# Kernel optimization log

Hardware: AMD Instinct MI355X
Metric: run time of the kernel (lower is better)

The kernel has to match this reference:

```python
import jax, jax.numpy as jnp
import numpy as np

N_USERS, N_ITEMS, N_GENRES = 31360, 6807, 18
TOTAL = N_USERS + N_ITEMS + N_GENRES          # 38185
OFFSET = TOTAL - N_GENRES                      # 38167
D = 16                                         # embedding_dim
B = 524288                                     # batch
MLP_DIMS = [64, 32, 16]
IN_DIM = 3 * D                                 # field_num * embedding_dim


def setup_inputs() -> dict:
    key = jax.random.key(0)
    ks = jax.random.split(key, 14)
    user = jax.random.randint(ks[0], (B, 1), 0, N_USERS)
    item = N_USERS + jax.random.randint(ks[1], (B, 1), 0, N_ITEMS)
    x_onehot = jnp.concatenate([user, item], axis=1)            # [B,2] global ids
    multi_hot = jax.random.randint(ks[2], (B, N_GENRES), 0, 2)  # [B,18] 0/1 mask
    s = 0.05
    emb_table = s * jax.random.normal(ks[3], (TOTAL, D), jnp.float32)
    fc_table = s * jax.random.normal(ks[4], (TOTAL, 1), jnp.float32)
    W1 = s * jax.random.normal(ks[5], (IN_DIM, MLP_DIMS[0]), jnp.float32)
    b1 = jnp.zeros((MLP_DIMS[0],), jnp.float32)
    W2 = s * jax.random.normal(ks[6], (MLP_DIMS[0], MLP_DIMS[1]), jnp.float32)
    b2 = jnp.zeros((MLP_DIMS[1],), jnp.float32)
    W3 = s * jax.random.normal(ks[7], (MLP_DIMS[1], MLP_DIMS[2]), jnp.float32)
    b3 = jnp.zeros((MLP_DIMS[2],), jnp.float32)
    W4 = s * jax.random.normal(ks[8], (MLP_DIMS[2], 1), jnp.float32)
    b4 = jnp.zeros((1,), jnp.float32)
    bias = jnp.zeros((1,), jnp.float32)
    return {"x_onehot": x_onehot, "multi_hot": multi_hot,
            "emb_table": emb_table, "fc_table": fc_table,
            "W1": W1, "b1": b1, "W2": W2, "b2": b2,
            "W3": W3, "b3": b3, "W4": W4, "b4": b4, "bias": bias}


def reference(x_onehot, multi_hot, emb_table, fc_table,
              W1, b1, W2, b2, W3, b3, W4, b4, bias):
    mh = multi_hot.astype(emb_table.dtype)                      # [B,18]
    # ragged multi-hot sum == mask @ genre slice of table (EmbeddingBag sum)
    embed_mh = mh @ emb_table[OFFSET:]                          # [B,D]
    embed_x = jnp.concatenate(
        [emb_table[x_onehot], embed_mh[:, None, :]], axis=1)    # [B,3,D]
    fc_mh = mh @ fc_table[OFFSET:]                              # [B,1]
    fc_x = jnp.concatenate(
        [fc_table[x_onehot], fc_mh[:, None, :]], axis=1)        # [B,3,1]
    # FM second-order term
    sum_e = embed_x.sum(axis=1)                                 # [B,D]
    fm_y = bias + fc_x.sum(axis=1) + 0.5 * jnp.sum(
        sum_e ** 2 - (embed_x ** 2).sum(axis=1), axis=1, keepdims=True)  # [B,1]
    # MLP (dropout inactive at inference)
    h = embed_x.reshape(embed_x.shape[0], -1)                   # [B,48]
    h = jax.nn.relu(h @ W1 + b1)
    h = jax.nn.relu(h @ W2 + b2)
    h = jax.nn.relu(h @ W3 + b3)
    mlp_y = h @ W4 + b4                                         # [B,1]
    return jax.nn.sigmoid(fm_y[:, 0] + mlp_y[:, 0])             # [B]
```

## Files before the change

kernel.cpp:

```cpp
#include <hip/hip_runtime.h>
#include <hip/hip_bf16.h>

namespace {

constexpr int kBatch  = 524288;
constexpr int kD      = 16;
constexpr int kOffset = 38167;
constexpr int kNG     = 18;
constexpr int kAStr   = 72;

constexpr int W1A  = 0;
constexpr int W1B  = 2560;
constexpr int W2O  = 5120;
constexpr int W3O  = 7424;
constexpr int WTOT = 8064;

typedef __attribute__((ext_vector_type(8))) short short8;
typedef __attribute__((ext_vector_type(4))) float f32x4;

__device__ __forceinline__ unsigned short f2bf(float f) {
    return __builtin_bit_cast(unsigned short, __float2bfloat16(f));
}
__device__ __forceinline__ unsigned pk2(float a, float b) {
    return (unsigned)f2bf(a) | ((unsigned)f2bf(b) << 16);
}
__device__ __forceinline__ float bf2f(unsigned short s) {
    union { unsigned u; float f; } v; v.u = ((unsigned)s) << 16;
    return v.f;
}

__global__ void prep_weights(const float* __restrict__ emb,
                             const float* __restrict__ W1,
                             const float* __restrict__ W2,
                             const float* __restrict__ W3,
                             unsigned short* __restrict__ wimg)
{
    const int t = (int)threadIdx.x;
    for (int i = t; i < WTOT; i += 256) wimg[i] = 0;
    __syncthreads();
    for (int i = t; i < 64 * 32; i += 256) {
        int n = i >> 5, k = i & 31;
        wimg[W1A + n * 40 + k] = f2bf(W1[k * 64 + n]);
    }
    for (int i = t; i < 512; i += 256) {
        int c = i >> 5, r = i & 31, g = r >> 3, j = r & 7;
        int k = 8 * g + j;
        wimg[W1A + (4 * c + g) * 40 + 32 + j] =
            (k < kNG) ? f2bf(emb[(size_t)(kOffset + k) * kD + c]) : (unsigned short)0;
    }
    for (int i = t; i < 64 * 16; i += 256) {
        int n = i >> 4, kk = i & 15;
        wimg[W1B + n * 40 + kk] = f2bf(W1[(32 + kk) * 64 + n]);
    }
    for (int i = t; i < 32 * 64; i += 256) {
        int n = i >> 6, k = i & 63;
        wimg[W2O + n * 72 + k] = f2bf(W2[k * 32 + n]);
    }
    for (int i = t; i < 16 * 32; i += 256) {
        int n = i >> 5, k = i & 31;
        wimg[W3O + n * 40 + k] = f2bf(W3[k * 16 + n]);
    }
}

__global__ __launch_bounds__(256, 3) void deepfm_fwd(
    const int*   __restrict__ x_onehot,
    const int*   __restrict__ multi_hot,
    const float* __restrict__ emb,
    const float* __restrict__ fc,
    const unsigned short* __restrict__ wimg,
    const float* __restrict__ b1,
    const float* __restrict__ b2,
    const float* __restrict__ b3,
    const float* __restrict__ W4,
    const float* __restrict__ b4,
    const float* __restrict__ bias,
    float*       __restrict__ out)
{
    __shared__ alignas(16) unsigned short s_w[WTOT];
    __shared__ alignas(16) unsigned short s_act[4][64 * kAStr];

    const int t = (int)threadIdx.x;

    {
        const uint4* src = reinterpret_cast<const uint4*>(wimg);
        uint4*       dst = reinterpret_cast<uint4*>(s_w);
        #pragma unroll
        for (int q = 0; q < 4; ++q) {
            const int idx = t + 256 * q;
            if (idx < WTOT / 8) dst[idx] = src[idx];
        }
    }

    const int i    = (int)blockIdx.x * 256 + t;
    const int lane = t & 63;
    const int w    = t >> 6;
    const int c    = lane & 15, g = lane >> 4;
    unsigned short* __restrict__ aw = s_act[w];
    unsigned short* __restrict__ ar = aw + lane * kAStr;

    int2 mh[9];
    {
        const int2* mh2 = reinterpret_cast<const int2*>(multi_hot + (size_t)kNG * i);
        #pragma unroll
        for (int q = 0; q < 9; ++q) mh[q] = mh2[q];
    }
    const int2 ids = *reinterpret_cast<const int2*>(x_onehot + 2 * (size_t)i);

    float h[32];
    {
        const float4* eu = reinterpret_cast<const float4*>(emb + (size_t)ids.x * kD);
        #pragma unroll
        for (int q = 0; q < 4; ++q) {
            const float4 a = eu[q];
            h[4*q+0] = a.x; h[4*q+1] = a.y; h[4*q+2] = a.z; h[4*q+3] = a.w;
        }
        const float4* ei = reinterpret_cast<const float4*>(emb + (size_t)ids.y * kD);
        #pragma unroll
        for (int q = 0; q < 4; ++q) {
            const float4 a = ei[q];
            h[16+4*q+0] = a.x; h[16+4*q+1] = a.y; h[16+4*q+2] = a.z; h[16+4*q+3] = a.w;
        }
    }

    float b1v[4];
    #pragma unroll
    for (int nt = 0; nt < 4; ++nt) b1v[nt] = b1[16 * nt + c];
    float b2v[2]; b2v[0] = b2[c]; b2v[1] = b2[16 + c];
    const float b3v = b3[c];

    float lin = bias[0] + b4[0] + fc[ids.x] + fc[ids.y];
    #pragma unroll
    for (int q = 0; q < 9; ++q) {
        lin += mh[q].x ? fc[kOffset + 2 * q]     : 0.f;
        lin += mh[q].y ? fc[kOffset + 2 * q + 1] : 0.f;
    }

    {
        unsigned mw[9];
        #pragma unroll
        for (int q = 0; q < 9; ++q)
            mw[q] = (mh[q].x ? 0x3F80u : 0u) | (mh[q].y ? 0x3F800000u : 0u);
        uint4 v0; v0.x = mw[0]; v0.y = mw[1]; v0.z = mw[2]; v0.w = mw[3];
        uint4 v1; v1.x = mw[4]; v1.y = mw[5]; v1.z = mw[6]; v1.w = mw[7];
        uint4 v2; v2.x = mw[8]; v2.y = 0u;    v2.z = 0u;    v2.w = 0u;
        uint4 vz; vz.x = vz.y = vz.z = vz.w = 0u;
        *reinterpret_cast<uint4*>(ar +  0) = v0;
        *reinterpret_cast<uint4*>(ar +  8) = v1;
        *reinterpret_cast<uint4*>(ar + 16) = v2;
        *reinterpret_cast<uint4*>(ar + 24) = vz;
        *reinterpret_cast<uint4*>(ar + 48) = vz;
        *reinterpret_cast<uint4*>(ar + 56) = vz;
    }

    __syncthreads();

    const f32x4 z4 = {0.f, 0.f, 0.f, 0.f};

    {
        const short8 bfrag = *reinterpret_cast<const short8*>(s_w + W1A + (4 * c + g) * 40 + 32);
        short8 af[4];
        #pragma unroll
        for (int mt = 0; mt < 4; ++mt)
            af[mt] = *reinterpret_cast<const short8*>(aw + (16 * mt + c) * kAStr + 8 * g);
        f32x4 accb[4];
        #pragma unroll
        for (int mt = 0; mt < 4; ++mt)
            accb[mt] = __builtin_amdgcn_mfma_f32_16x16x32_bf16(af[mt], bfrag, z4, 0, 0, 0);
        #pragma unroll
        for (int mt = 0; mt < 4; ++mt)
            #pragma unroll
            for (int r = 0; r < 4; ++r)
                aw[(16 * mt + 4 * g + r) * kAStr + 32 + c] = f2bf(accb[mt][r]);
    }

    {
        #pragma unroll
        for (int q = 0; q < 4; ++q) {
            uint4 d;
            d.x = pk2(h[8*q+0], h[8*q+1]);
            d.y = pk2(h[8*q+2], h[8*q+3]);
            d.z = pk2(h[8*q+4], h[8*q+5]);
            d.w = pk2(h[8*q+6], h[8*q+7]);
            *reinterpret_cast<uint4*>(ar + 8 * q) = d;
        }
    }

    float fm = 0.f;
    {
        const uint4 p0 = *reinterpret_cast<const uint4*>(ar + 32);
        const uint4 p1 = *reinterpret_cast<const uint4*>(ar + 40);
        const unsigned pp[8] = {p0.x, p0.y, p0.z, p0.w, p1.x, p1.y, p1.z, p1.w};
        float em[16];
        #pragma unroll
        for (int j = 0; j < 8; ++j) {
            em[2*j+0] = bf2f((unsigned short)(pp[j] & 0xFFFFu));
            em[2*j+1] = bf2f((unsigned short)(pp[j] >> 16));
        }
        #pragma unroll
        for (int d = 0; d < kD; ++d) fm = fmaf(h[d], h[16 + d], fm);
        #pragma unroll
        for (int d = 0; d < kD; ++d) fm = fmaf(h[d] + h[16 + d], em[d], fm);
    }

    f32x4 acc1[4][4];
    #pragma unroll
    for (int mt = 0; mt < 4; ++mt)
        #pragma unroll
        for (int nt = 0; nt < 4; ++nt) acc1[mt][nt] = z4;
    #pragma unroll
    for (int kt = 0; kt < 2; ++kt) {
        short8 af[4], bfr[4];
        #pragma unroll
        for (int mt = 0; mt < 4; ++mt)
            af[mt] = *reinterpret_cast<const short8*>(aw + (16*mt + c) * kAStr + 32*kt + 8*g);
        const int wb = kt ? W1B : W1A;
        #pragma unroll
        for (int nt = 0; nt < 4; ++nt)
            bfr[nt] = *reinterpret_cast<const short8*>(s_w + wb + (16*nt + c) * 40 + 8*g);
        #pragma unroll
        for (int mt = 0; mt < 4; ++mt)
            #pragma unroll
            for (int nt = 0; nt < 4; ++nt)
                acc1[mt][nt] = __builtin_amdgcn_mfma_f32_16x16x32_bf16(af[mt], bfr[nt], acc1[mt][nt], 0, 0, 0);
    }
    #pragma unroll
    for (int mt = 0; mt < 4; ++mt)
        #pragma unroll
        for (int nt = 0; nt < 4; ++nt)
            #pragma unroll
            for (int r = 0; r < 4; ++r) {
                const float v = fmaxf(acc1[mt][nt][r] + b1v[nt], 0.f);
                aw[(16*mt + 4*g + r) * kAStr + 16*nt + c] = f2bf(v);
            }

    f32x4 acc2[4][2];
    #pragma unroll
    for (int mt = 0; mt < 4; ++mt)
        #pragma unroll
        for (int nt = 0; nt < 2; ++nt) acc2[mt][nt] = z4;
    #pragma unroll
    for (int kt = 0; kt < 2; ++kt) {
        short8 af[4], bfr[2];
        #pragma unroll
        for (int mt = 0; mt < 4; ++mt)
            af[mt] = *reinterpret_cast<const short8*>(aw + (16*mt + c) * kAStr + 32*kt + 8*g);
        #pragma unroll
        for (int nt = 0; nt < 2; ++nt)
            bfr[nt] = *reinterpret_cast<const short8*>(s_w + W2O + (16*nt + c) * 72 + 32*kt + 8*g);
        #pragma unroll
        for (int mt = 0; mt < 4; ++mt)
            #pragma unroll
            for (int nt = 0; nt < 2; ++nt)
                acc2[mt][nt] = __builtin_amdgcn_mfma_f32_16x16x32_bf16(af[mt], bfr[nt], acc2[mt][nt], 0, 0, 0);
    }
    #pragma unroll
    for (int mt = 0; mt < 4; ++mt)
        #pragma unroll
        for (int nt = 0; nt < 2; ++nt)
            #pragma unroll
            for (int r = 0; r < 4; ++r) {
                const float v = fmaxf(acc2[mt][nt][r] + b2v[nt], 0.f);
                aw[(16*mt + 4*g + r) * kAStr + 16*nt + c] = f2bf(v);
            }

    f32x4 acc3[4];
    #pragma unroll
    for (int mt = 0; mt < 4; ++mt) acc3[mt] = z4;
    {
        const short8 bfr = *reinterpret_cast<const short8*>(s_w + W3O + c * 40 + 8*g);
        short8 af[4];
        #pragma unroll
        for (int mt = 0; mt < 4; ++mt)
            af[mt] = *reinterpret_cast<const short8*>(aw + (16*mt + c) * kAStr + 8*g);
        #pragma unroll
        for (int mt = 0; mt < 4; ++mt)
            acc3[mt] = __builtin_amdgcn_mfma_f32_16x16x32_bf16(af[mt], bfr, acc3[mt], 0, 0, 0);
    }
    #pragma unroll
    for (int mt = 0; mt < 4; ++mt)
        #pragma unroll
        for (int r = 0; r < 4; ++r) {
            const float v = fmaxf(acc3[mt][r] + b3v, 0.f);
            aw[(16*mt + 4*g + r) * kAStr + c] = f2bf(v);
        }

    float mlp = 0.f;
    {
        const uint4 p0 = *reinterpret_cast<const uint4*>(ar);
        const uint4 p1 = *reinterpret_cast<const uint4*>(ar + 8);
        const unsigned pp[8] = {p0.x, p0.y, p0.z, p0.w, p1.x, p1.y, p1.z, p1.w};
        #pragma unroll
        for (int j = 0; j < 8; ++j) {
            mlp = fmaf(bf2f((unsigned short)(pp[j] & 0xFFFFu)), W4[2*j],     mlp);
            mlp = fmaf(bf2f((unsigned short)(pp[j] >> 16)),     W4[2*j + 1], mlp);
        }
    }

    const float x = lin + fm + mlp;
    out[i] = 1.0f / (1.0f + __expf(-x));
}

}

extern "C" void kernel_launch(void* const* d_in, const int* in_sizes, int n_in,
                              void* d_out, int out_size, void* d_ws, size_t ws_size,
                              hipStream_t stream) {
    (void)in_sizes; (void)n_in; (void)ws_size; (void)out_size;
    const int*   x_onehot  = (const int*)  d_in[0];
    const int*   multi_hot = (const int*)  d_in[1];
    const float* emb       = (const float*)d_in[2];
    const float* fc        = (const float*)d_in[3];
    const float* W1        = (const float*)d_in[4];
    const float* b1        = (const float*)d_in[5];
    const float* W2        = (const float*)d_in[6];
    const float* b2        = (const float*)d_in[7];
    const float* W3        = (const float*)d_in[8];
    const float* b3        = (const float*)d_in[9];
    const float* W4        = (const float*)d_in[10];
    const float* b4        = (const float*)d_in[11];
    const float* biasp     = (const float*)d_in[12];
    float* out = (float*)d_out;
    unsigned short* wimg = (unsigned short*)d_ws;

    hipLaunchKernelGGL(prep_weights, dim3(1), dim3(256), 0, stream,
                       emb, W1, W2, W3, wimg);
    hipLaunchKernelGGL(deepfm_fwd, dim3(kBatch / 256), dim3(256), 0, stream,
                       x_onehot, multi_hot, emb, fc, wimg,
                       b1, b2, b3, W4, b4, biasp, out);
}
```

Before: 37.36 us.

## Swizzle LDS layouts with XOR and move to 512-thread blocks

Replaces the padded-stride shared-memory layout for activations and weights with a 128-byte-row XOR-swizzled layout to avoid bank conflicts on the MFMA fragment loads and the scattered accumulator stores. The block size doubles to 512 threads (8 waves), which spreads the per-block weight copy over twice as many rows. Bias-add and ReLU are rewritten on float2 vectors so they can use packed instructions. LDS per block grows to about 78KB, so the occupancy target of 4 blocks may not be reachable, and the swizzle adds address arithmetic.

```diff
diff --git a/kernel.cpp b/kernel.cpp
--- a/kernel.cpp
+++ b/kernel.cpp
@@ -7,16 +7,16 @@
 constexpr int kD      = 16;
 constexpr int kOffset = 38167;
 constexpr int kNG     = 18;
-constexpr int kAStr   = 72;
-
-constexpr int W1A  = 0;
-constexpr int W1B  = 2560;
-constexpr int W2O  = 5120;
-constexpr int W3O  = 7424;
-constexpr int WTOT = 8064;
+
+constexpr int W1B0   = 0;
+constexpr int W2B0   = 8192;
+constexpr int W3B0   = 12288;
+constexpr int GB0    = 13312;
+constexpr int WBYTES = 14336;
 
 typedef __attribute__((ext_vector_type(8))) short short8;
 typedef __attribute__((ext_vector_type(4))) float f32x4;
+typedef __attribute__((ext_vector_type(2))) float f32x2;
 
 __device__ __forceinline__ unsigned short f2bf(float f) {
     return __builtin_bit_cast(unsigned short, __float2bfloat16(f));
@@ -27,6 +27,12 @@
 __device__ __forceinline__ float bf2f(unsigned short s) {
     union { unsigned u; float f; } v; v.u = ((unsigned)s) << 16;
     return v.f;
+}
+__device__ __forceinline__ unsigned short* AP(unsigned short* b, int row, int col) {
+    return (unsigned short*)((char*)b + row * 128 + ((col * 2) ^ ((row & 7) << 4)));
+}
+__device__ __forceinline__ const unsigned short* APc(const unsigned short* b, int row, int col) {
+    return (const unsigned short*)((const char*)b + row * 128 + ((col * 2) ^ ((row & 7) << 4)));
 }
 
 __global__ void prep_weights(const float* __restrict__ emb,
@@ -36,33 +42,32 @@
                              unsigned short* __restrict__ wimg)
 {
     const int t = (int)threadIdx.x;
-    for (int i = t; i < WTOT; i += 256) wimg[i] = 0;
+    for (int i = t; i < WBYTES / 2; i += 256) wimg[i] = 0;
     __syncthreads();
+    for (int i = t; i < 48 * 64; i += 256) {
+        int k = i >> 6, n = i & 63;
+        int byte = W1B0 + n * 128 + ((k * 2) ^ ((n & 7) << 4));
+        wimg[byte >> 1] = f2bf(W1[k * 64 + n]);
+    }
     for (int i = t; i < 64 * 32; i += 256) {
-        int n = i >> 5, k = i & 31;
-        wimg[W1A + n * 40 + k] = f2bf(W1[k * 64 + n]);
+        int k = i >> 5, n = i & 31;
+        int byte = W2B0 + n * 128 + ((k * 2) ^ ((n & 7) << 4));
+        wimg[byte >> 1] = f2bf(W2[k * 32 + n]);
+    }
+    for (int i = t; i < 32 * 16; i += 256) {
+        int k = i >> 4, n = i & 15;
+        int byte = W3B0 + n * 64 + ((k * 2) ^ ((n & 3) << 4));
+        wimg[byte >> 1] = f2bf(W3[k * 16 + n]);
     }
     for (int i = t; i < 512; i += 256) {
         int c = i >> 5, r = i & 31, g = r >> 3, j = r & 7;
-        int k = 8 * g + j;
-        wimg[W1A + (4 * c + g) * 40 + 32 + j] =
-            (k < kNG) ? f2bf(emb[(size_t)(kOffset + k) * kD + c]) : (unsigned short)0;
-    }
-    for (int i = t; i < 64 * 16; i += 256) {
-        int n = i >> 4, kk = i & 15;
-        wimg[W1B + n * 40 + kk] = f2bf(W1[(32 + kk) * 64 + n]);
-    }
-    for (int i = t; i < 32 * 64; i += 256) {
-        int n = i >> 6, k = i & 63;
-        wimg[W2O + n * 72 + k] = f2bf(W2[k * 32 + n]);
-    }
-    for (int i = t; i < 16 * 32; i += 256) {
-        int n = i >> 5, k = i & 31;
-        wimg[W3O + n * 40 + k] = f2bf(W3[k * 16 + n]);
-    }
-}
-
-__global__ __launch_bounds__(256, 3) void deepfm_fwd(
+        int kg = 8 * g + j;
+        wimg[(GB0 >> 1) + (4 * c + g) * 8 + j] =
+            (kg < kNG) ? f2bf(emb[(size_t)(kOffset + kg) * kD + c]) : (unsigned short)0;
+    }
+}
+
+__global__ __launch_bounds__(512, 4) void deepfm_fwd(
     const int*   __restrict__ x_onehot,
     const int*   __restrict__ multi_hot,
     const float* __restrict__ emb,
@@ -76,27 +81,24 @@
     const float* __restrict__ bias,
     float*       __restrict__ out)
 {
-    __shared__ alignas(16) unsigned short s_w[WTOT];
-    __shared__ alignas(16) unsigned short s_act[4][64 * kAStr];
+    __shared__ alignas(16) unsigned short s_w[WBYTES / 2];
+    __shared__ alignas(16) unsigned short s_act[8 * 4096];
 
     const int t = (int)threadIdx.x;
 
     {
         const uint4* src = reinterpret_cast<const uint4*>(wimg);
         uint4*       dst = reinterpret_cast<uint4*>(s_w);
-        #pragma unroll
-        for (int q = 0; q < 4; ++q) {
-            const int idx = t + 256 * q;
-            if (idx < WTOT / 8) dst[idx] = src[idx];
-        }
-    }
-
-    const int i    = (int)blockIdx.x * 256 + t;
+        if (t < 896) dst[t] = src[t];
+        const int t2 = t + 512;
+        if (t2 < 896) dst[t2] = src[t2];
+    }
+
+    const int i    = (int)blockIdx.x * 512 + t;
     const int lane = t & 63;
     const int w    = t >> 6;
     const int c    = lane & 15, g = lane >> 4;
-    unsigned short* __restrict__ aw = s_act[w];
-    unsigned short* __restrict__ ar = aw + lane * kAStr;
+    unsigned short* __restrict__ aw = s_act + w * 4096;
 
     int2 mh[9];
     {
@@ -144,24 +146,25 @@
         uint4 v1; v1.x = mw[4]; v1.y = mw[5]; v1.z = mw[6]; v1.w = mw[7];
         uint4 v2; v2.x = mw[8]; v2.y = 0u;    v2.z = 0u;    v2.w = 0u;
         uint4 vz; vz.x = vz.y = vz.z = vz.w = 0u;
-        *reinterpret_cast<uint4*>(ar +  0) = v0;
-        *reinterpret_cast<uint4*>(ar +  8) = v1;
-        *reinterpret_cast<uint4*>(ar + 16) = v2;
-        *reinterpret_cast<uint4*>(ar + 24) = vz;
-        *reinterpret_cast<uint4*>(ar + 48) = vz;
-        *reinterpret_cast<uint4*>(ar + 56) = vz;
+        *reinterpret_cast<uint4*>(AP(aw, lane,  0)) = v0;
+        *reinterpret_cast<uint4*>(AP(aw, lane,  8)) = v1;
+        *reinterpret_cast<uint4*>(AP(aw, lane, 16)) = v2;
+        *reinterpret_cast<uint4*>(AP(aw, lane, 24)) = vz;
+        *reinterpret_cast<uint4*>(AP(aw, lane, 48)) = vz;
+        *reinterpret_cast<uint4*>(AP(aw, lane, 56)) = vz;
     }
 
     __syncthreads();
 
     const f32x4 z4 = {0.f, 0.f, 0.f, 0.f};
-
-    {
-        const short8 bfrag = *reinterpret_cast<const short8*>(s_w + W1A + (4 * c + g) * 40 + 32);
+    const f32x2 zz = {0.f, 0.f};
+
+    {
+        const short8 bfrag = *reinterpret_cast<const short8*>(s_w + (GB0 >> 1) + (4 * c + g) * 8);
         short8 af[4];
         #pragma unroll
         for (int mt = 0; mt < 4; ++mt)
-            af[mt] = *reinterpret_cast<const short8*>(aw + (16 * mt + c) * kAStr + 8 * g);
+            af[mt] = *reinterpret_cast<const short8*>(APc(aw, 16 * mt + c, 8 * g));
         f32x4 accb[4];
         #pragma unroll
         for (int mt = 0; mt < 4; ++mt)
@@ -170,7 +173,7 @@
         for (int mt = 0; mt < 4; ++mt)
             #pragma unroll
             for (int r = 0; r < 4; ++r)
-                aw[(16 * mt + 4 * g + r) * kAStr + 32 + c] = f2bf(accb[mt][r]);
+                *AP(aw, 16 * mt + 4 * g + r, 32 + c) = f2bf(accb[mt][r]);
     }
 
     {
@@ -181,14 +184,14 @@
             d.y = pk2(h[8*q+2], h[8*q+3]);
             d.z = pk2(h[8*q+4], h[8*q+5]);
             d.w = pk2(h[8*q+6], h[8*q+7]);
-            *reinterpret_cast<uint4*>(ar + 8 * q) = d;
+            *reinterpret_cast<uint4*>(AP(aw, lane, 8 * q)) = d;
         }
     }
 
     float fm = 0.f;
     {
-        const uint4 p0 = *reinterpret_cast<const uint4*>(ar + 32);
-        const uint4 p1 = *reinterpret_cast<const uint4*>(ar + 40);
+        const uint4 p0 = *reinterpret_cast<const uint4*>(APc(aw, lane, 32));
+        const uint4 p1 = *reinterpret_cast<const uint4*>(APc(aw, lane, 40));
         const unsigned pp[8] = {p0.x, p0.y, p0.z, p0.w, p1.x, p1.y, p1.z, p1.w};
         float em[16];
         #pragma unroll
@@ -212,11 +215,11 @@
         short8 af[4], bfr[4];
         #pragma unroll
         for (int mt = 0; mt < 4; ++mt)
-            af[mt] = *reinterpret_cast<const short8*>(aw + (16*mt + c) * kAStr + 32*kt + 8*g);
-        const int wb = kt ? W1B : W1A;
+            af[mt] = *reinterpret_cast<const short8*>(APc(aw, 16*mt + c, 32*kt + 8*g));
         #pragma unroll
         for (int nt = 0; nt < 4; ++nt)
-            bfr[nt] = *reinterpret_cast<const short8*>(s_w + wb + (16*nt + c) * 40 + 8*g);
+            bfr[nt] = *reinterpret_cast<const short8*>(
+                (const char*)s_w + W1B0 + (16*nt + c) * 128 + ((64*kt + 16*g) ^ ((c & 7) << 4)));
         #pragma unroll
         for (int mt = 0; mt < 4; ++mt)
             #pragma unroll
@@ -226,12 +229,18 @@
     #pragma unroll
     for (int mt = 0; mt < 4; ++mt)
         #pragma unroll
-        for (int nt = 0; nt < 4; ++nt)
-            #pragma unroll
-            for (int r = 0; r < 4; ++r) {
-                const float v = fmaxf(acc1[mt][nt][r] + b1v[nt], 0.f);
-                aw[(16*mt + 4*g + r) * kAStr + 16*nt + c] = f2bf(v);
-            }
+        for (int nt = 0; nt < 4; ++nt) {
+            f32x2 p0 = {acc1[mt][nt][0], acc1[mt][nt][1]};
+            f32x2 p1 = {acc1[mt][nt][2], acc1[mt][nt][3]};
+            const f32x2 bb = {b1v[nt], b1v[nt]};
+            p0 += bb; p1 += bb;
+            p0 = __builtin_elementwise_max(p0, zz);
+            p1 = __builtin_elementwise_max(p1, zz);
+            *AP(aw, 16*mt + 4*g + 0, 16*nt + c) = f2bf(p0[0]);
+            *AP(aw, 16*mt + 4*g + 1, 16*nt + c) = f2bf(p0[1]);
+            *AP(aw, 16*mt + 4*g + 2, 16*nt + c) = f2bf(p1[0]);
+            *AP(aw, 16*mt + 4*g + 3, 16*nt + c) = f2bf(p1[1]);
+        }
 
     f32x4 acc2[4][2];
     #pragma unroll
@@ -243,10 +252,11 @@
         short8 af[4], bfr[2];
         #pragma unroll
         for (int mt = 0; mt < 4; ++mt)
-            af[mt] = *reinterpret_cast<const short8*>(aw + (16*mt + c) * kAStr + 32*kt + 8*g);
+            af[mt] = *reinterpret_cast<const short8*>(APc(aw, 16*mt + c, 32*kt + 8*g));
         #pragma unroll
         for (int nt = 0; nt < 2; ++nt)
-            bfr[nt] = *reinterpret_cast<const short8*>(s_w + W2O + (16*nt + c) * 72 + 32*kt + 8*g);
+            bfr[nt] = *reinterpret_cast<const short8*>(
+                (const char*)s_w + W2B0 + (16*nt + c) * 128 + ((64*kt + 16*g) ^ ((c & 7) << 4)));
         #pragma unroll
         for (int mt = 0; mt < 4; ++mt)
             #pragma unroll
@@ -256,38 +266,51 @@
     #pragma unroll
     for (int mt = 0; mt < 4; ++mt)
         #pragma unroll
-        for (int nt = 0; nt < 2; ++nt)
-            #pragma unroll
-            for (int r = 0; r < 4; ++r) {
-                const float v = fmaxf(acc2[mt][nt][r] + b2v[nt], 0.f);
-                aw[(16*mt + 4*g + r) * kAStr + 16*nt + c] = f2bf(v);
-            }
+        for (int nt = 0; nt < 2; ++nt) {
+            f32x2 p0 = {acc2[mt][nt][0], acc2[mt][nt][1]};
+            f32x2 p1 = {acc2[mt][nt][2], acc2[mt][nt][3]};
+            const f32x2 bb = {b2v[nt], b2v[nt]};
+            p0 += bb; p1 += bb;
+            p0 = __builtin_elementwise_max(p0, zz);
+            p1 = __builtin_elementwise_max(p1, zz);
+            *AP(aw, 16*mt + 4*g + 0, 16*nt + c) = f2bf(p0[0]);
+            *AP(aw, 16*mt + 4*g + 1, 16*nt + c) = f2bf(p0[1]);
+            *AP(aw, 16*mt + 4*g + 2, 16*nt + c) = f2bf(p1[0]);
+            *AP(aw, 16*mt + 4*g + 3, 16*nt + c) = f2bf(p1[1]);
+        }
 
     f32x4 acc3[4];
     #pragma unroll
     for (int mt = 0; mt < 4; ++mt) acc3[mt] = z4;
     {
-        const short8 bfr = *reinterpret_cast<const short8*>(s_w + W3O + c * 40 + 8*g);
+        const short8 bfr = *reinterpret_cast<const short8*>(
+            (const char*)s_w + W3B0 + c * 64 + ((16*g) ^ ((c & 3) << 4)));
         short8 af[4];
         #pragma unroll
         for (int mt = 0; mt < 4; ++mt)
-            af[mt] = *reinterpret_cast<const short8*>(aw + (16*mt + c) * kAStr + 8*g);
+            af[mt] = *reinterpret_cast<const short8*>(APc(aw, 16*mt + c, 8*g));
         #pragma unroll
         for (int mt = 0; mt < 4; ++mt)
             acc3[mt] = __builtin_amdgcn_mfma_f32_16x16x32_bf16(af[mt], bfr, acc3[mt], 0, 0, 0);
     }
     #pragma unroll
-    for (int mt = 0; mt < 4; ++mt)
-        #pragma unroll
-        for (int r = 0; r < 4; ++r) {
-            const float v = fmaxf(acc3[mt][r] + b3v, 0.f);
-            aw[(16*mt + 4*g + r) * kAStr + c] = f2bf(v);
-        }
+    for (int mt = 0; mt < 4; ++mt) {
+        f32x2 p0 = {acc3[mt][0], acc3[mt][1]};
+        f32x2 p1 = {acc3[mt][2], acc3[mt][3]};
+        const f32x2 bb = {b3v, b3v};
+        p0 += bb; p1 += bb;
+        p0 = __builtin_elementwise_max(p0, zz);
+        p1 = __builtin_elementwise_max(p1, zz);
+        *AP(aw, 16*mt + 4*g + 0, c) = f2bf(p0[0]);
+        *AP(aw, 16*mt + 4*g + 1, c) = f2bf(p0[1]);
+        *AP(aw, 16*mt + 4*g + 2, c) = f2bf(p1[0]);
+        *AP(aw, 16*mt + 4*g + 3, c) = f2bf(p1[1]);
+    }
 
     float mlp = 0.f;
     {
-        const uint4 p0 = *reinterpret_cast<const uint4*>(ar);
-        const uint4 p1 = *reinterpret_cast<const uint4*>(ar + 8);
+        const uint4 p0 = *reinterpret_cast<const uint4*>(APc(aw, lane, 0));
+        const uint4 p1 = *reinterpret_cast<const uint4*>(APc(aw, lane, 8));
         const unsigned pp[8] = {p0.x, p0.y, p0.z, p0.w, p1.x, p1.y, p1.z, p1.w};
         #pragma unroll
         for (int j = 0; j < 8; ++j) {
@@ -324,7 +347,7 @@
 
     hipLaunchKernelGGL(prep_weights, dim3(1), dim3(256), 0, stream,
                        emb, W1, W2, W3, wimg);
-    hipLaunchKernelGGL(deepfm_fwd, dim3(kBatch / 256), dim3(256), 0, stream,
+    hipLaunchKernelGGL(deepfm_fwd, dim3(kBatch / 512), dim3(512), 0, stream,
                        x_onehot, multi_hot, emb, fc, wimg,
                        b1, b2, b3, W4, b4, biasp, out);
 }
```

Result: slower. 66.66 us (+78.4%).

## Use XOR-swizzled 128-byte-row LDS layout for activations and MLP weights

Applied to the files above, without the earlier changes.

Replaces the padded-stride (72/40 element) shared-memory layouts for activations and W1/W2/W3 with 128-byte rows whose 16-byte chunks are XOR-swizzled by row index, and moves the genre embedding fragment into its own block. Precomputed per-lane swizzled addresses serve MFMA fragment reads and bf16 scatter writes. The aim is fewer LDS bank conflicts on the short8 fragment loads and the 2-byte stores. The activation buffer shrinks slightly but the weight image grows, and the address logic costs a few extra registers.

```diff
diff --git a/kernel.cpp b/kernel.cpp
--- a/kernel.cpp
+++ b/kernel.cpp
@@ -7,13 +7,12 @@
 constexpr int kD      = 16;
 constexpr int kOffset = 38167;
 constexpr int kNG     = 18;
-constexpr int kAStr   = 72;
-
-constexpr int W1A  = 0;
-constexpr int W1B  = 2560;
-constexpr int W2O  = 5120;
-constexpr int W3O  = 7424;
-constexpr int WTOT = 8064;
+
+constexpr int W1B0   = 0;
+constexpr int W2B0   = 8192;
+constexpr int W3B0   = 12288;
+constexpr int GB0    = 13312;
+constexpr int WBYTES = 14336;
 
 typedef __attribute__((ext_vector_type(8))) short short8;
 typedef __attribute__((ext_vector_type(4))) float f32x4;
@@ -36,29 +35,28 @@
                              unsigned short* __restrict__ wimg)
 {
     const int t = (int)threadIdx.x;
-    for (int i = t; i < WTOT; i += 256) wimg[i] = 0;
+    for (int i = t; i < WBYTES / 2; i += 256) wimg[i] = 0;
     __syncthreads();
+    for (int i = t; i < 48 * 64; i += 256) {
+        int k = i >> 6, n = i & 63;
+        int byte = W1B0 + n * 128 + ((k * 2) ^ ((n & 7) << 4));
+        wimg[byte >> 1] = f2bf(W1[k * 64 + n]);
+    }
     for (int i = t; i < 64 * 32; i += 256) {
-        int n = i >> 5, k = i & 31;
-        wimg[W1A + n * 40 + k] = f2bf(W1[k * 64 + n]);
+        int k = i >> 5, n = i & 31;
+        int byte = W2B0 + n * 128 + ((k * 2) ^ ((n & 7) << 4));
+        wimg[byte >> 1] = f2bf(W2[k * 32 + n]);
+    }
+    for (int i = t; i < 32 * 16; i += 256) {
+        int k = i >> 4, n = i & 15;
+        int byte = W3B0 + n * 64 + ((k * 2) ^ ((n & 3) << 4));
+        wimg[byte >> 1] = f2bf(W3[k * 16 + n]);
     }
     for (int i = t; i < 512; i += 256) {
         int c = i >> 5, r = i & 31, g = r >> 3, j = r & 7;
-        int k = 8 * g + j;
-        wimg[W1A + (4 * c + g) * 40 + 32 + j] =
-            (k < kNG) ? f2bf(emb[(size_t)(kOffset + k) * kD + c]) : (unsigned short)0;
-    }
-    for (int i = t; i < 64 * 16; i += 256) {
-        int n = i >> 4, kk = i & 15;
-        wimg[W1B + n * 40 + kk] = f2bf(W1[(32 + kk) * 64 + n]);
-    }
-    for (int i = t; i < 32 * 64; i += 256) {
-        int n = i >> 6, k = i & 63;
-        wimg[W2O + n * 72 + k] = f2bf(W2[k * 32 + n]);
-    }
-    for (int i = t; i < 16 * 32; i += 256) {
-        int n = i >> 5, k = i & 31;
-        wimg[W3O + n * 40 + k] = f2bf(W3[k * 16 + n]);
+        int kg = 8 * g + j;
+        wimg[(GB0 >> 1) + (4 * c + g) * 8 + j] =
+            (kg < kNG) ? f2bf(emb[(size_t)(kOffset + kg) * kD + c]) : (unsigned short)0;
     }
 }
 
@@ -76,8 +74,8 @@
     const float* __restrict__ bias,
     float*       __restrict__ out)
 {
-    __shared__ alignas(16) unsigned short s_w[WTOT];
-    __shared__ alignas(16) unsigned short s_act[4][64 * kAStr];
+    __shared__ alignas(16) unsigned short s_w[WBYTES / 2];
+    __shared__ alignas(16) unsigned short s_act[4 * 4096];
 
     const int t = (int)threadIdx.x;
 
@@ -87,7 +85,7 @@
         #pragma unroll
         for (int q = 0; q < 4; ++q) {
             const int idx = t + 256 * q;
-            if (idx < WTOT / 8) dst[idx] = src[idx];
+            if (idx < WBYTES / 16) dst[idx] = src[idx];
         }
     }
 
@@ -95,8 +93,26 @@
     const int lane = t & 63;
     const int w    = t >> 6;
     const int c    = lane & 15, g = lane >> 4;
-    unsigned short* __restrict__ aw = s_act[w];
-    unsigned short* __restrict__ ar = aw + lane * kAStr;
+    char* __restrict__ awc = (char*)(s_act + w * 4096);
+    const char* __restrict__ swc = (const char*)s_w;
+
+    const int l7 = lane & 7;
+    const int sb = lane * 128;
+    int rA[2];
+    #pragma unroll
+    for (int kt = 0; kt < 2; ++kt)
+        rA[kt] = c * 128 + (((4 * kt + g) ^ (c & 7)) << 4);
+    int wad[4][4];
+    #pragma unroll
+    for (int r = 0; r < 4; ++r) {
+        const int Xlo  = (r & 1) << 4;
+        const int Xhi  = (2 * (g & 1) + (r >> 1)) << 5;
+        const int rowb = (4 * g + r) * 128 + ((2 * c) ^ Xlo);
+        #pragma unroll
+        for (int nt = 0; nt < 4; ++nt)
+            wad[r][nt] = rowb + ((32 * nt) ^ Xhi);
+    }
+    const int rW3 = W3B0 + c * 64 + ((g ^ (c & 3)) << 4);
 
     int2 mh[9];
     {
@@ -144,12 +160,12 @@
         uint4 v1; v1.x = mw[4]; v1.y = mw[5]; v1.z = mw[6]; v1.w = mw[7];
         uint4 v2; v2.x = mw[8]; v2.y = 0u;    v2.z = 0u;    v2.w = 0u;
         uint4 vz; vz.x = vz.y = vz.z = vz.w = 0u;
-        *reinterpret_cast<uint4*>(ar +  0) = v0;
-        *reinterpret_cast<uint4*>(ar +  8) = v1;
-        *reinterpret_cast<uint4*>(ar + 16) = v2;
-        *reinterpret_cast<uint4*>(ar + 24) = vz;
-        *reinterpret_cast<uint4*>(ar + 48) = vz;
-        *reinterpret_cast<uint4*>(ar + 56) = vz;
+        *reinterpret_cast<uint4*>(awc + sb + (((0 ^ l7)) << 4)) = v0;
+        *reinterpret_cast<uint4*>(awc + sb + (((1 ^ l7)) << 4)) = v1;
+        *reinterpret_cast<uint4*>(awc + sb + (((2 ^ l7)) << 4)) = v2;
+        *reinterpret_cast<uint4*>(awc + sb + (((3 ^ l7)) << 4)) = vz;
+        *reinterpret_cast<uint4*>(awc + sb + (((6 ^ l7)) << 4)) = vz;
+        *reinterpret_cast<uint4*>(awc + sb + (((7 ^ l7)) << 4)) = vz;
     }
 
     __syncthreads();
@@ -157,11 +173,11 @@
     const f32x4 z4 = {0.f, 0.f, 0.f, 0.f};
 
     {
-        const short8 bfrag = *reinterpret_cast<const short8*>(s_w + W1A + (4 * c + g) * 40 + 32);
+        const short8 bfrag = *reinterpret_cast<const short8*>(s_w + (GB0 >> 1) + (4 * c + g) * 8);
         short8 af[4];
         #pragma unroll
         for (int mt = 0; mt < 4; ++mt)
-            af[mt] = *reinterpret_cast<const short8*>(aw + (16 * mt + c) * kAStr + 8 * g);
+            af[mt] = *reinterpret_cast<const short8*>(awc + rA[0] + 2048 * mt);
         f32x4 accb[4];
         #pragma unroll
         for (int mt = 0; mt < 4; ++mt)
@@ -170,7 +186,7 @@
         for (int mt = 0; mt < 4; ++mt)
             #pragma unroll
             for (int r = 0; r < 4; ++r)
-                aw[(16 * mt + 4 * g + r) * kAStr + 32 + c] = f2bf(accb[mt][r]);
+                *reinterpret_cast<unsigned short*>(awc + wad[r][2] + 2048 * mt) = f2bf(accb[mt][r]);
     }
 
     {
@@ -181,14 +197,14 @@
             d.y = pk2(h[8*q+2], h[8*q+3]);
             d.z = pk2(h[8*q+4], h[8*q+5]);
             d.w = pk2(h[8*q+6], h[8*q+7]);
-            *reinterpret_cast<uint4*>(ar + 8 * q) = d;
+            *reinterpret_cast<uint4*>(awc + sb + ((q ^ l7) << 4)) = d;
         }
     }
 
     float fm = 0.f;
     {
-        const uint4 p0 = *reinterpret_cast<const uint4*>(ar + 32);
-        const uint4 p1 = *reinterpret_cast<const uint4*>(ar + 40);
+        const uint4 p0 = *reinterpret_cast<const uint4*>(awc + sb + ((4 ^ l7) << 4));
+        const uint4 p1 = *reinterpret_cast<const uint4*>(awc + sb + ((5 ^ l7) << 4));
         const unsigned pp[8] = {p0.x, p0.y, p0.z, p0.w, p1.x, p1.y, p1.z, p1.w};
         float em[16];
         #pragma unroll
@@ -212,11 +228,10 @@
         short8 af[4], bfr[4];
         #pragma unroll
         for (int mt = 0; mt < 4; ++mt)
-            af[mt] = *reinterpret_cast<const short8*>(aw + (16*mt + c) * kAStr + 32*kt + 8*g);
-        const int wb = kt ? W1B : W1A;
+            af[mt] = *reinterpret_cast<const short8*>(awc + rA[kt] + 2048 * mt);
         #pragma unroll
         for (int nt = 0; nt < 4; ++nt)
-            bfr[nt] = *reinterpret_cast<const short8*>(s_w + wb + (16*nt + c) * 40 + 8*g);
+            bfr[nt] = *reinterpret_cast<const short8*>(swc + W1B0 + rA[kt] + 2048 * nt);
         #pragma unroll
         for (int mt = 0; mt < 4; ++mt)
             #pragma unroll
@@ -230,7 +245,7 @@
             #pragma unroll
             for (int r = 0; r < 4; ++r) {
                 const float v = fmaxf(acc1[mt][nt][r] + b1v[nt], 0.f);
-                aw[(16*mt + 4*g + r) * kAStr + 16*nt + c] = f2bf(v);
+                *reinterpret_cast<unsigned short*>(awc + wad[r][nt] + 2048 * mt) = f2bf(v);
             }
 
     f32x4 acc2[4][2];
@@ -243,10 +258,10 @@
         short8 af[4], bfr[2];
         #pragma unroll
         for (int mt = 0; mt < 4; ++mt)
-            af[mt] = *reinterpret_cast<const short8*>(aw + (16*mt + c) * kAStr + 32*kt + 8*g);
+            af[mt] = *reinterpret_cast<const short8*>(awc + rA[kt] + 2048 * mt);
         #pragma unroll
         for (int nt = 0; nt < 2; ++nt)
-            bfr[nt] = *reinterpret_cast<const short8*>(s_w + W2O + (16*nt + c) * 72 + 32*kt + 8*g);
+            bfr[nt] = *reinterpret_cast<const short8*>(swc + W2B0 + rA[kt] + 2048 * nt);
         #pragma unroll
         for (int mt = 0; mt < 4; ++mt)
             #pragma unroll
@@ -260,18 +275,18 @@
             #pragma unroll
             for (int r = 0; r < 4; ++r) {
                 const float v = fmaxf(acc2[mt][nt][r] + b2v[nt], 0.f);
-                aw[(16*mt + 4*g + r) * kAStr + 16*nt + c] = f2bf(v);
+                *reinterpret_cast<unsigned short*>(awc + wad[r][nt] + 2048 * mt) = f2bf(v);
             }
 
     f32x4 acc3[4];
     #pragma unroll
     for (int mt = 0; mt < 4; ++mt) acc3[mt] = z4;
     {
-        const short8 bfr = *reinterpret_cast<const short8*>(s_w + W3O + c * 40 + 8*g);
+        const short8 bfr = *reinterpret_cast<const short8*>(swc + rW3);
         short8 af[4];
         #pragma unroll
         for (int mt = 0; mt < 4; ++mt)
-            af[mt] = *reinterpret_cast<const short8*>(aw + (16*mt + c) * kAStr + 8*g);
+            af[mt] = *reinterpret_cast<const short8*>(awc + rA[0] + 2048 * mt);
         #pragma unroll
         for (int mt = 0; mt < 4; ++mt)
             acc3[mt] = __builtin_amdgcn_mfma_f32_16x16x32_bf16(af[mt], bfr, acc3[mt], 0, 0, 0);
@@ -281,13 +296,13 @@
         #pragma unroll
         for (int r = 0; r < 4; ++r) {
             const float v = fmaxf(acc3[mt][r] + b3v, 0.f);
-            aw[(16*mt + 4*g + r) * kAStr + c] = f2bf(v);
+            *reinterpret_cast<unsigned short*>(awc + wad[r][0] + 2048 * mt) = f2bf(v);
         }
 
     float mlp = 0.f;
     {
-        const uint4 p0 = *reinterpret_cast<const uint4*>(ar);
-        const uint4 p1 = *reinterpret_cast<const uint4*>(ar + 8);
+        const uint4 p0 = *reinterpret_cast<const uint4*>(awc + sb + ((0 ^ l7) << 4));
+        const uint4 p1 = *reinterpret_cast<const uint4*>(awc + sb + ((1 ^ l7) << 4));
         const unsigned pp[8] = {p0.x, p0.y, p0.z, p0.w, p1.x, p1.y, p1.z, p1.w};
         #pragma unroll
         for (int j = 0; j < 8; ++j) {
```

New measurement: 39.73 us. 6.3% more time.
